# Kernel optimization log

Hardware: AMD Instinct MI355X
Metric: run time of the kernel (lower is better)

## Reference

```python
import math
import jax, jax.numpy as jnp
import numpy as np

HIDDEN = 2048
N_HEADS = 16
N_KV_HEADS = 4
HEAD_DIM = HIDDEN // N_HEADS  # 128
SEQ = 2048
BATCH = 2
RMS_EPS = 1.1920928955078125e-07  # torch float32 eps (nn.RMSNorm default eps=None)


def setup_inputs() -> dict:
    key = jax.random.key(0)
    ks = jax.random.split(key, 8)
    x = jax.random.normal(ks[0], (BATCH, SEQ, HIDDEN), dtype=jnp.float32)
    # RoPE tables, half-rotation layout: [f0..f_{d/2-1}, f0..f_{d/2-1}]
    inv_freq = 1.0 / (10000.0 ** (jnp.arange(0, HEAD_DIM, 2, dtype=jnp.float32) / HEAD_DIM))
    t = jnp.arange(SEQ, dtype=jnp.float32)
    freqs = jnp.outer(t, inv_freq)                      # [S, D/2]
    emb = jnp.concatenate([freqs, freqs], axis=-1)      # [S, D]
    sin, cos = jnp.sin(emb), jnp.cos(emb)
    s = 0.02
    Wq = jax.random.normal(ks[1], (HIDDEN, HIDDEN), dtype=jnp.float32) * s
    Wk = jax.random.normal(ks[2], (HIDDEN, N_KV_HEADS * HEAD_DIM), dtype=jnp.float32) * s
    Wv = jax.random.normal(ks[3], (HIDDEN, N_KV_HEADS * HEAD_DIM), dtype=jnp.float32) * s
    Wo = jax.random.normal(ks[4], (HIDDEN, HIDDEN), dtype=jnp.float32) * s
    q_norm_w = jnp.ones((HEAD_DIM,), dtype=jnp.float32)
    k_norm_w = jnp.ones((HEAD_DIM,), dtype=jnp.float32)
    return {"x": x, "sin": sin, "cos": cos, "Wq": Wq, "Wk": Wk, "Wv": Wv,
            "Wo": Wo, "q_norm_w": q_norm_w, "k_norm_w": k_norm_w}


def _rms_norm(t, w):
    # RMSNorm over last dim (head_dim) with learned weight
    var = jnp.mean(t * t, axis=-1, keepdims=True)
    return t * jax.lax.rsqrt(var + RMS_EPS) * w


def _apply_rope(t, sin, cos):
    # t: [B, H, S, D]; sin/cos: [S, D] broadcast
    half = t.shape[-1] // 2
    rotated = jnp.concatenate([-t[..., half:], t[..., :half]], axis=-1)
    return cos * t + sin * rotated


def reference(x, sin, cos, Wq, Wk, Wv, Wo, q_norm_w, k_norm_w):
    b, s, _ = x.shape
    rep = N_HEADS // N_KV_HEADS
    # Q: proj -> norm -> transpose -> rope
    q = (x @ Wq).reshape(b, s, N_HEADS, HEAD_DIM)
    q = _rms_norm(q, q_norm_w).transpose(0, 2, 1, 3)           # [B, H, S, D]
    q = _apply_rope(q, sin, cos)
    # K: proj -> repeat kv heads -> norm -> transpose -> rope
    k = (x @ Wk).reshape(b, s, N_KV_HEADS, HEAD_DIM)
    k = jnp.repeat(k, rep, axis=2)                              # [B, S, H, D]
    k = _rms_norm(k, k_norm_w).transpose(0, 2, 1, 3)            # [B, H, S, D]
    k = _apply_rope(k, sin, cos)
    # V: proj -> repeat kv heads -> transpose
    v = (x @ Wv).reshape(b, s, N_KV_HEADS, HEAD_DIM)
    v = jnp.repeat(v, rep, axis=2).transpose(0, 2, 1, 3)        # [B, H, S, D]
    # explicit masked softmax attention (materializes [B,H,S,S])
    scores = jnp.einsum('bhqd,bhkd->bhqk', q, k) / math.sqrt(HEAD_DIM)
    causal = jnp.triu(jnp.ones((s, s), dtype=bool), 1)
    scores = jnp.where(causal, -jnp.inf, scores)
    attn = jax.nn.softmax(scores, axis=-1)
    o = jnp.einsum('bhqk,bhkd->bhqd', attn, v)                  # [B, H, S, D]
    o = o.transpose(0, 2, 1, 3).reshape(b, s, HIDDEN)
    return o @ Wo
```

## Files before the change

### kernel.cpp

```cpp
#include <hip/hip_runtime.h>

typedef __attribute__((ext_vector_type(8))) short bf16x8;
typedef __attribute__((ext_vector_type(4))) short bf16x4;
typedef __attribute__((ext_vector_type(4))) float f32x4;

#define HIDDEN 2048
#define NH 16
#define NKV 4
#define HD 128
#define SEQ_N 2048
#define NT 4096
#define QKV_N 3072
#define RMS_EPS 1.1920928955078125e-07f
#define QSCALE 0.08838834764831845f
#define SM_C 12.0f

static __device__ __forceinline__ float b2f(unsigned short u) {
  union { unsigned int i; float f; } v; v.i = ((unsigned int)u) << 16; return v.f;
}
static __device__ __forceinline__ unsigned short f2b(float f) {
  union { float f; unsigned int i; } v; v.f = f;
  unsigned int r = (v.i + 0x7fffu + ((v.i >> 16) & 1u)) >> 16;
  return (unsigned short)r;
}
static __device__ __forceinline__ void gload_lds16(const unsigned short* g, unsigned short* l) {
  __builtin_amdgcn_global_load_lds(
      (const __attribute__((address_space(1))) unsigned int*)g,
      (__attribute__((address_space(3))) unsigned int*)l, 16, 0, 0);
}
static __device__ __forceinline__ void store_c(float* p, float v) { *p = v; }
static __device__ __forceinline__ void store_c(unsigned short* p, float v) { *p = f2b(v); }

template <typename OutT>
__device__ __forceinline__ void gemm_tile(
    const unsigned short* __restrict__ A, int lda,
    const unsigned short* __restrict__ BT, int ldb,
    OutT* __restrict__ C, int ldc,
    int K, int m0, int nloc0, int nout0) {
  __shared__ unsigned short As[4096], Bs[4096];
  const int tid  = threadIdx.x;
  const int wid  = tid >> 6, lane = tid & 63;
  const int g    = lane >> 4, cc = lane & 15;
  const int wr   = wid >> 1,  wc = wid & 1;
  const int r0   = tid >> 2;
  const int cb0  = (tid & 3) * 8;

  f32x4 acc[4][4];
#pragma unroll
  for (int i = 0; i < 4; ++i)
#pragma unroll
    for (int j = 0; j < 4; ++j) acc[i][j] = (f32x4){0.f, 0.f, 0.f, 0.f};

  unsigned short* AsW0 = As + wid * 512;
  unsigned short* AsW1 = As + 2048 + wid * 512;
  unsigned short* BsW0 = Bs + wid * 512;
  unsigned short* BsW1 = Bs + 2048 + wid * 512;
  const unsigned short* Ab0 = A  + (size_t)(m0 + r0)        * lda + cb0;
  const unsigned short* Ab1 = A  + (size_t)(m0 + 64 + r0)   * lda + cb0;
  const unsigned short* Bb0 = BT + (size_t)(nloc0 + r0)     * ldb + cb0;
  const unsigned short* Bb1 = BT + (size_t)(nloc0 + 64 + r0)* ldb + cb0;

  for (int kt = 0; kt < K; kt += 32) {
    gload_lds16(Ab0 + kt, AsW0);
    gload_lds16(Ab1 + kt, AsW1);
    gload_lds16(Bb0 + kt, BsW0);
    gload_lds16(Bb1 + kt, BsW1);
    __syncthreads();
    bf16x8 af[4], bfr[4];
#pragma unroll
    for (int mi = 0; mi < 4; ++mi)
      af[mi] = *(const bf16x8*)(As + ((wr * 64 + mi * 16 + cc) * 32 + g * 8));
#pragma unroll
    for (int ni = 0; ni < 4; ++ni)
      bfr[ni] = *(const bf16x8*)(Bs + ((wc * 64 + ni * 16 + cc) * 32 + g * 8));
#pragma unroll
    for (int mi = 0; mi < 4; ++mi)
#pragma unroll
      for (int ni = 0; ni < 4; ++ni)
        acc[mi][ni] = __builtin_amdgcn_mfma_f32_16x16x32_bf16(af[mi], bfr[ni], acc[mi][ni], 0, 0, 0);
    __syncthreads();
  }
#pragma unroll
  for (int mi = 0; mi < 4; ++mi)
#pragma unroll
    for (int ni = 0; ni < 4; ++ni)
#pragma unroll
      for (int j = 0; j < 4; ++j) {
        int row = m0 + wr * 64 + mi * 16 + g * 4 + j;
        int col = nout0 + wc * 64 + ni * 16 + cc;
        store_c(&C[(size_t)row * ldc + col], acc[mi][ni][j]);
      }
}

__global__ __launch_bounds__(256) void k_gemm_qkv(
    const unsigned short* __restrict__ x,
    const unsigned short* __restrict__ WqT,
    const unsigned short* __restrict__ WkT,
    const unsigned short* __restrict__ WvT,
    unsigned short* __restrict__ Praw) {
  int wg = (blockIdx.x & 7) * 96 + (blockIdx.x >> 3);
  int nb = wg % 24, mb = wg / 24;
  int n0 = nb * 128;
  const unsigned short* BT; int nloc;
  if (n0 < HIDDEN)            { BT = WqT; nloc = n0; }
  else if (n0 < HIDDEN + 512) { BT = WkT; nloc = n0 - HIDDEN; }
  else                        { BT = WvT; nloc = n0 - (HIDDEN + 512); }
  gemm_tile<unsigned short>(x, HIDDEN, BT, HIDDEN, Praw, QKV_N, HIDDEN, mb * 128, nloc, n0);
}

__global__ __launch_bounds__(256) void k_gemm_o(
    const unsigned short* __restrict__ Oa,
    const unsigned short* __restrict__ WoT,
    float* __restrict__ out) {
  int wg = (blockIdx.x & 7) * 64 + (blockIdx.x >> 3);
  int nb = wg % 16, mb = wg / 16;
  gemm_tile<float>(Oa, HIDDEN, WoT, HIDDEN, out, HIDDEN, HIDDEN, mb * 128, nb * 128, nb * 128);
}

__global__ __launch_bounds__(256) void k_cvt_f2b(
    const float* __restrict__ src, unsigned short* __restrict__ dst) {
  int i = (blockIdx.x * 256 + threadIdx.x) * 8;
  float4 a = *(const float4*)(src + i);
  float4 b = *(const float4*)(src + i + 4);
  bf16x8 v;
  v[0] = (short)f2b(a.x); v[1] = (short)f2b(a.y); v[2] = (short)f2b(a.z); v[3] = (short)f2b(a.w);
  v[4] = (short)f2b(b.x); v[5] = (short)f2b(b.y); v[6] = (short)f2b(b.z); v[7] = (short)f2b(b.w);
  *(bf16x8*)(dst + i) = v;
}

__global__ __launch_bounds__(256) void k_transpose_f2b(
    const float* __restrict__ src, unsigned short* __restrict__ dst,
    int ld_src, int ld_dst, int tilesC) {
  __shared__ float T[64][68];
  int tr = blockIdx.x / tilesC, tc = blockIdx.x % tilesC;
  int r0 = tr * 64, c0 = tc * 64;
  int tid = threadIdx.x;
#pragma unroll
  for (int it = 0; it < 4; ++it) {
    int u = it * 256 + tid;
    int r = u >> 4, cb = (u & 15) * 4;
    float4 v = *(const float4*)(src + (size_t)(r0 + r) * ld_src + c0 + cb);
    T[r][cb] = v.x; T[r][cb + 1] = v.y; T[r][cb + 2] = v.z; T[r][cb + 3] = v.w;
  }
  __syncthreads();
#pragma unroll
  for (int it = 0; it < 2; ++it) {
    int u = it * 256 + tid;
    int dc = u >> 3, rb = (u & 7) * 8;
    bf16x8 v;
#pragma unroll
    for (int j = 0; j < 8; ++j) v[j] = (short)f2b(T[rb + j][dc]);
    *(bf16x8*)(dst + (size_t)(c0 + dc) * ld_dst + r0 + rb) = v;
  }
}

__global__ __launch_bounds__(256) void k_transpose_bb(
    const unsigned short* __restrict__ src, unsigned short* __restrict__ dst,
    int ld_src, int ld_dst, int tilesC) {
  __shared__ unsigned short T[64][80];
  int tr = blockIdx.x / tilesC, tc = blockIdx.x % tilesC;
  int r0 = tr * 64, c0 = tc * 64;
  int tid = threadIdx.x;
#pragma unroll
  for (int it = 0; it < 2; ++it) {
    int u = it * 256 + tid; int r = u >> 3, cb = (u & 7) * 8;
    bf16x8 v = *(const bf16x8*)(src + (size_t)(r0 + r) * ld_src + c0 + cb);
    *(bf16x8*)(&T[r][cb]) = v;
  }
  __syncthreads();
#pragma unroll
  for (int it = 0; it < 2; ++it) {
    int u = it * 256 + tid; int dc = u >> 3, rb = (u & 7) * 8;
    bf16x8 v;
#pragma unroll
    for (int j = 0; j < 8; ++j) v[j] = (short)T[rb + j][dc];
    *(bf16x8*)(dst + (size_t)(c0 + dc) * ld_dst + r0 + rb) = v;
  }
}

__global__ __launch_bounds__(256) void k_qk_post(
    const unsigned short* __restrict__ Praw,
    const float* __restrict__ sinT,
    const float* __restrict__ cosT,
    const float* __restrict__ qw,
    const float* __restrict__ kw,
    unsigned short* __restrict__ Qbuf,
    unsigned short* __restrict__ Kbuf) {
  int sub = threadIdx.x >> 4;
  int sl  = threadIdx.x & 15;
  int rid = blockIdx.x * 16 + sub;
  int t = rid / 20, slot = rid - t * 20;
  int b = t >> 11, s = t & 2047;
  const int isq = (slot < 16);
  int cb = isq ? slot * 128 : HIDDEN + (slot - 16) * 128;
  const unsigned short* src = Praw + (size_t)t * QKV_N + cb;
  const int d0 = sl * 4;
  bf16x4 a0 = *(const bf16x4*)(src + d0);
  bf16x4 a1 = *(const bf16x4*)(src + 64 + d0);
  float x0[4], x1[4];
  float ssq = 0.f;
#pragma unroll
  for (int j = 0; j < 4; ++j) {
    x0[j] = b2f((unsigned short)a0[j]);
    x1[j] = b2f((unsigned short)a1[j]);
    ssq += x0[j] * x0[j] + x1[j] * x1[j];
  }
#pragma unroll
  for (int mk = 1; mk < 16; mk <<= 1) ssq += __shfl_xor(ssq, mk, 64);
  float r = rsqrtf(ssq * (1.0f / 128.0f) + RMS_EPS);
  const float* w = isq ? qw : kw;
  f32x4 w0 = *(const f32x4*)(w + d0);
  f32x4 w1 = *(const f32x4*)(w + 64 + d0);
  f32x4 cs0 = *(const f32x4*)(cosT + s * 128 + d0);
  f32x4 cs1 = *(const f32x4*)(cosT + s * 128 + 64 + d0);
  f32x4 sn0 = *(const f32x4*)(sinT + s * 128 + d0);
  f32x4 sn1 = *(const f32x4*)(sinT + s * 128 + 64 + d0);
  unsigned short* dst = isq
      ? Qbuf + ((size_t)(b * NH + slot) * SEQ_N + s) * HD
      : Kbuf + ((size_t)(b * NKV + (slot - 16)) * SEQ_N + s) * HD;
  const float qs = isq ? QSCALE : 1.0f;
  bf16x4 o0, o1;
#pragma unroll
  for (int j = 0; j < 4; ++j) {
    float n0 = x0[j] * r * w0[j];
    float n1 = x1[j] * r * w1[j];
    o0[j] = (short)f2b((cs0[j] * n0 - sn0[j] * n1) * qs);
    o1[j] = (short)f2b((cs1[j] * n1 + sn1[j] * n0) * qs);
  }
  *(bf16x4*)(dst + d0) = o0;
  *(bf16x4*)(dst + 64 + d0) = o1;
}

__global__ __launch_bounds__(256, 2) void k_attn(
    const unsigned short* __restrict__ Q,
    const unsigned short* __restrict__ K,
    const unsigned short* __restrict__ V,
    unsigned short* __restrict__ O) {
  __shared__ unsigned short Ks[2][64 * 128];
  __shared__ unsigned short Vs[2][128 * 64];
  __shared__ unsigned short Ps[4][16 * 64];
  const int tid = threadIdx.x, wid = tid >> 6, lane = tid & 63;
  const int g = lane >> 4, c = lane & 15;
  const int bid = blockIdx.x;
  const int bh = bid & 31;
  const int b = bh >> 4, h = bh & 15;
  const int z = bid >> 5;
  const int zz = z & 7, zr = z >> 3;
  const int qt = (zr == 0) ? zz : (zr == 1) ? 15 - zz : (zr == 2) ? 16 + zz : 31 - zz;
  const int wq0 = qt * 64 + wid * 16;
  const int kv = h >> 2;
  const int nt = qt + 1;

  const unsigned short* Qp = Q + (size_t)(b * NH + h) * SEQ_N * HD;
  const unsigned short* Kp = K + (size_t)(b * NKV + kv) * SEQ_N * HD;
  const unsigned short* Vp = V + (size_t)(kv * HD) * NT + b * SEQ_N;

  const int krow_l = lane >> 4;
  const int kcol_l = (lane & 15) * 8;
  const int vrow_l = lane >> 3;
  const int vcol_l = (lane & 7) * 8;

  bf16x8 qfr[4];
#pragma unroll
  for (int ks = 0; ks < 4; ++ks)
    qfr[ks] = *(const bf16x8*)(Qp + (size_t)(wq0 + c) * HD + ks * 32 + g * 8);

  f32x4 o[8];
#pragma unroll
  for (int df = 0; df < 8; ++df) o[df] = (f32x4){0.f, 0.f, 0.f, 0.f};
  float l_i[4] = {0.f, 0.f, 0.f, 0.f};

#define STAGE(BUF, KBASE)                                                          \
  {                                                                                \
    _Pragma("unroll")                                                              \
    for (int ch = 0; ch < 4; ++ch) {                                               \
      int chunk = wid * 4 + ch;                                                    \
      int rk = chunk * 4 + krow_l;                                                 \
      int ck = kcol_l ^ ((rk & 15) << 3);                                          \
      gload_lds16(Kp + (size_t)((KBASE) + rk) * HD + ck, &Ks[BUF][chunk * 512]);   \
      int rv = chunk * 8 + vrow_l;                                                 \
      int cv = vcol_l ^ ((rv & 7) << 3);                                           \
      gload_lds16(Vp + (size_t)rv * NT + (KBASE) + cv, &Vs[BUF][chunk * 512]);     \
    }                                                                              \
  }

  int buf = 0;
  STAGE(0, 0);
  __syncthreads();

  for (int kt = 0; kt < nt; ++kt) {
    const int kbase = kt * 64;
    if (kt + 1 < nt) STAGE(buf ^ 1, kbase + 64);

    f32x4 s[4];
#pragma unroll
    for (int kf = 0; kf < 4; ++kf) s[kf] = (f32x4){0.f, 0.f, 0.f, 0.f};
    __builtin_amdgcn_s_setprio(1);
#pragma unroll
    for (int ks = 0; ks < 4; ++ks) {
      bf16x8 bk[4];
#pragma unroll
      for (int kf = 0; kf < 4; ++kf) {
        int r = kf * 16 + c;
        int e = (ks * 32 + g * 8) ^ ((r & 15) << 3);
        bk[kf] = *(const bf16x8*)(&Ks[buf][r * 128 + e]);
      }
#pragma unroll
      for (int kf = 0; kf < 4; ++kf)
        s[kf] = __builtin_amdgcn_mfma_f32_16x16x32_bf16(qfr[ks], bk[kf], s[kf], 0, 0, 0);
    }
    __builtin_amdgcn_s_setprio(0);
    if (kbase + 63 > wq0) {
#pragma unroll
      for (int kf = 0; kf < 4; ++kf)
#pragma unroll
        for (int i = 0; i < 4; ++i) {
          int q = wq0 + g * 4 + i;
          int kp = kbase + kf * 16 + c;
          if (kp > q) s[kf][i] = -1e30f;
        }
    }
#pragma unroll
    for (int kf = 0; kf < 4; ++kf)
#pragma unroll
      for (int i = 0; i < 4; ++i) {
        float p = __expf(s[kf][i] - SM_C);
        l_i[i] += p;
        int r = g * 4 + i;
        int e = (kf * 16 + c) ^ ((r & 7) << 3);
        Ps[wid][r * 64 + e] = f2b(p);
      }
    __builtin_amdgcn_s_setprio(1);
#pragma unroll
    for (int ksp = 0; ksp < 2; ++ksp) {
      int ep = (ksp * 32 + g * 8) ^ ((c & 7) << 3);
      bf16x8 pa = *(const bf16x8*)(&Ps[wid][c * 64 + ep]);
#pragma unroll
      for (int df = 0; df < 8; ++df) {
        int rv = df * 16 + c;
        int e = (ksp * 32 + g * 8) ^ ((rv & 7) << 3);
        bf16x8 vb = *(const bf16x8*)(&Vs[buf][rv * 64 + e]);
        o[df] = __builtin_amdgcn_mfma_f32_16x16x32_bf16(pa, vb, o[df], 0, 0, 0);
      }
    }
    __builtin_amdgcn_s_setprio(0);
    __syncthreads();
    buf ^= 1;
  }

  unsigned short* Op = O + (size_t)(b * SEQ_N) * HIDDEN + h * HD;
#pragma unroll
  for (int i = 0; i < 4; ++i) {
    float t = l_i[i];
    t += __shfl_xor(t, 1, 64);
    t += __shfl_xor(t, 2, 64);
    t += __shfl_xor(t, 4, 64);
    t += __shfl_xor(t, 8, 64);
    float inv = 1.0f / t;
    int q = wq0 + g * 4 + i;
#pragma unroll
    for (int df = 0; df < 8; ++df)
      Op[(size_t)q * HIDDEN + df * 16 + c] = f2b(o[df][i] * inv);
  }
#undef STAGE
}

extern "C" void kernel_launch(void* const* d_in, const int* in_sizes, int n_in,
                              void* d_out, int out_size, void* d_ws, size_t ws_size,
                              hipStream_t stream) {
  const float* x    = (const float*)d_in[0];
  const float* sinT = (const float*)d_in[1];
  const float* cosT = (const float*)d_in[2];
  const float* Wq   = (const float*)d_in[3];
  const float* Wk   = (const float*)d_in[4];
  const float* Wv   = (const float*)d_in[5];
  const float* Wo   = (const float*)d_in[6];
  const float* qw   = (const float*)d_in[7];
  const float* kw   = (const float*)d_in[8];
  float* out = (float*)d_out;
  unsigned short* ws = (unsigned short*)d_ws;

  unsigned short* Xb   = ws;
  unsigned short* WqT  = ws + 8388608;
  unsigned short* WkT  = ws + 12582912;
  unsigned short* WvT  = ws + 13631488;
  unsigned short* WoT  = ws + 14680064;
  unsigned short* Praw = ws + 18874368;
  unsigned short* Qbuf = ws + 31457280;
  unsigned short* Kbuf = ws + 39845888;
  unsigned short* Vt   = ws + 41943040;
  unsigned short* Oatt = ws + 44040192;

  dim3 blk(256);
  k_cvt_f2b<<<4096, blk, 0, stream>>>(x, Xb);
  k_transpose_f2b<<<1024, blk, 0, stream>>>(Wq, WqT, 2048, 2048, 32);
  k_transpose_f2b<<<256,  blk, 0, stream>>>(Wk, WkT, 512,  2048, 8);
  k_transpose_f2b<<<256,  blk, 0, stream>>>(Wv, WvT, 512,  2048, 8);
  k_transpose_f2b<<<1024, blk, 0, stream>>>(Wo, WoT, 2048, 2048, 32);
  k_gemm_qkv<<<768, blk, 0, stream>>>(Xb, WqT, WkT, WvT, Praw);
  k_qk_post<<<5120, blk, 0, stream>>>(Praw, sinT, cosT, qw, kw, Qbuf, Kbuf);
  k_transpose_bb<<<512, blk, 0, stream>>>(Praw + 2560, Vt, 3072, 4096, 8);
  k_attn<<<1024, blk, 0, stream>>>(Qbuf, Kbuf, Vt, Oatt);
  k_gemm_o<<<512, blk, 0, stream>>>(Oatt, WoT, out);
}
```

Measured before the change: 321.0 us.

## Load K/V directly from global in attention, merge weight transposes, use exp2

The attention kernel drops its double-buffered LDS staging of K and V, along with the barriers and setprio hints, and reads MFMA operands straight from global memory through L1/L2. The four weight-transpose launches become one kernel that picks its matrix by block index. The softmax exponent is rewritten as exp2 of an FMA with log2(e) folded into the constants. Each attention operand load now goes to global memory, and four waves share each K/V tile, so the kernel depends more on cache hits and memory latency in exchange for dropping the LDS copies and barriers.

```diff
diff --git a/kernel.cpp b/kernel.cpp
--- a/kernel.cpp
+++ b/kernel.cpp
@@ -13,7 +13,8 @@
 #define QKV_N 3072
 #define RMS_EPS 1.1920928955078125e-07f
 #define QSCALE 0.08838834764831845f
-#define SM_C 12.0f
+#define SM_L2E 1.4426950408889634f
+#define SM_C2  17.312340490667562f
 
 static __device__ __forceinline__ float b2f(unsigned short u) {
   union { unsigned int i; float f; } v; v.i = ((unsigned int)u) << 16; return v.f;
@@ -128,11 +129,20 @@
   *(bf16x8*)(dst + i) = v;
 }
 
-__global__ __launch_bounds__(256) void k_transpose_f2b(
-    const float* __restrict__ src, unsigned short* __restrict__ dst,
-    int ld_src, int ld_dst, int tilesC) {
+__global__ __launch_bounds__(256) void k_transpose_all(
+    const float* __restrict__ Wq, const float* __restrict__ Wk,
+    const float* __restrict__ Wv, const float* __restrict__ Wo,
+    unsigned short* __restrict__ WqT, unsigned short* __restrict__ WkT,
+    unsigned short* __restrict__ WvT, unsigned short* __restrict__ WoT) {
   __shared__ float T[64][68];
-  int tr = blockIdx.x / tilesC, tc = blockIdx.x % tilesC;
+  int bid = blockIdx.x;
+  const float* src; unsigned short* dst; int ld_src, tilesC, tile;
+  if (bid < 1024)      { src = Wq; dst = WqT; ld_src = 2048; tilesC = 32; tile = bid; }
+  else if (bid < 1280) { src = Wk; dst = WkT; ld_src = 512;  tilesC = 8;  tile = bid - 1024; }
+  else if (bid < 1536) { src = Wv; dst = WvT; ld_src = 512;  tilesC = 8;  tile = bid - 1280; }
+  else                 { src = Wo; dst = WoT; ld_src = 2048; tilesC = 32; tile = bid - 1536; }
+  const int ld_dst = 2048;
+  int tr = tile / tilesC, tc = tile % tilesC;
   int r0 = tr * 64, c0 = tc * 64;
   int tid = threadIdx.x;
 #pragma unroll
@@ -231,13 +241,11 @@
   *(bf16x4*)(dst + 64 + d0) = o1;
 }
 
-__global__ __launch_bounds__(256, 2) void k_attn(
+__global__ __launch_bounds__(256) void k_attn(
     const unsigned short* __restrict__ Q,
     const unsigned short* __restrict__ K,
     const unsigned short* __restrict__ V,
     unsigned short* __restrict__ O) {
-  __shared__ unsigned short Ks[2][64 * 128];
-  __shared__ unsigned short Vs[2][128 * 64];
   __shared__ unsigned short Ps[4][16 * 64];
   const int tid = threadIdx.x, wid = tid >> 6, lane = tid & 63;
   const int g = lane >> 4, c = lane & 15;
@@ -255,11 +263,6 @@
   const unsigned short* Kp = K + (size_t)(b * NKV + kv) * SEQ_N * HD;
   const unsigned short* Vp = V + (size_t)(kv * HD) * NT + b * SEQ_N;
 
-  const int krow_l = lane >> 4;
-  const int kcol_l = (lane & 15) * 8;
-  const int vrow_l = lane >> 3;
-  const int vcol_l = (lane & 7) * 8;
-
   bf16x8 qfr[4];
 #pragma unroll
   for (int ks = 0; ks < 4; ++ks)
@@ -270,46 +273,22 @@
   for (int df = 0; df < 8; ++df) o[df] = (f32x4){0.f, 0.f, 0.f, 0.f};
   float l_i[4] = {0.f, 0.f, 0.f, 0.f};
 
-#define STAGE(BUF, KBASE)                                                          \
-  {                                                                                \
-    _Pragma("unroll")                                                              \
-    for (int ch = 0; ch < 4; ++ch) {                                               \
-      int chunk = wid * 4 + ch;                                                    \
-      int rk = chunk * 4 + krow_l;                                                 \
-      int ck = kcol_l ^ ((rk & 15) << 3);                                          \
-      gload_lds16(Kp + (size_t)((KBASE) + rk) * HD + ck, &Ks[BUF][chunk * 512]);   \
-      int rv = chunk * 8 + vrow_l;                                                 \
-      int cv = vcol_l ^ ((rv & 7) << 3);                                           \
-      gload_lds16(Vp + (size_t)rv * NT + (KBASE) + cv, &Vs[BUF][chunk * 512]);     \
-    }                                                                              \
-  }
-
-  int buf = 0;
-  STAGE(0, 0);
-  __syncthreads();
-
   for (int kt = 0; kt < nt; ++kt) {
     const int kbase = kt * 64;
-    if (kt + 1 < nt) STAGE(buf ^ 1, kbase + 64);
 
     f32x4 s[4];
 #pragma unroll
     for (int kf = 0; kf < 4; ++kf) s[kf] = (f32x4){0.f, 0.f, 0.f, 0.f};
-    __builtin_amdgcn_s_setprio(1);
 #pragma unroll
     for (int ks = 0; ks < 4; ++ks) {
       bf16x8 bk[4];
 #pragma unroll
-      for (int kf = 0; kf < 4; ++kf) {
-        int r = kf * 16 + c;
-        int e = (ks * 32 + g * 8) ^ ((r & 15) << 3);
-        bk[kf] = *(const bf16x8*)(&Ks[buf][r * 128 + e]);
-      }
+      for (int kf = 0; kf < 4; ++kf)
+        bk[kf] = *(const bf16x8*)(Kp + (size_t)(kbase + kf * 16 + c) * HD + ks * 32 + g * 8);
 #pragma unroll
       for (int kf = 0; kf < 4; ++kf)
         s[kf] = __builtin_amdgcn_mfma_f32_16x16x32_bf16(qfr[ks], bk[kf], s[kf], 0, 0, 0);
     }
-    __builtin_amdgcn_s_setprio(0);
     if (kbase + 63 > wq0) {
 #pragma unroll
       for (int kf = 0; kf < 4; ++kf)
@@ -324,28 +303,22 @@
     for (int kf = 0; kf < 4; ++kf)
 #pragma unroll
       for (int i = 0; i < 4; ++i) {
-        float p = __expf(s[kf][i] - SM_C);
+        float p = exp2f(fmaf(s[kf][i], SM_L2E, -SM_C2));
         l_i[i] += p;
         int r = g * 4 + i;
         int e = (kf * 16 + c) ^ ((r & 7) << 3);
         Ps[wid][r * 64 + e] = f2b(p);
       }
-    __builtin_amdgcn_s_setprio(1);
 #pragma unroll
     for (int ksp = 0; ksp < 2; ++ksp) {
       int ep = (ksp * 32 + g * 8) ^ ((c & 7) << 3);
       bf16x8 pa = *(const bf16x8*)(&Ps[wid][c * 64 + ep]);
 #pragma unroll
       for (int df = 0; df < 8; ++df) {
-        int rv = df * 16 + c;
-        int e = (ksp * 32 + g * 8) ^ ((rv & 7) << 3);
-        bf16x8 vb = *(const bf16x8*)(&Vs[buf][rv * 64 + e]);
+        bf16x8 vb = *(const bf16x8*)(Vp + (size_t)(df * 16 + c) * NT + kbase + ksp * 32 + g * 8);
         o[df] = __builtin_amdgcn_mfma_f32_16x16x32_bf16(pa, vb, o[df], 0, 0, 0);
       }
     }
-    __builtin_amdgcn_s_setprio(0);
-    __syncthreads();
-    buf ^= 1;
   }
 
   unsigned short* Op = O + (size_t)(b * SEQ_N) * HIDDEN + h * HD;
@@ -362,7 +335,6 @@
     for (int df = 0; df < 8; ++df)
       Op[(size_t)q * HIDDEN + df * 16 + c] = f2b(o[df][i] * inv);
   }
-#undef STAGE
 }
 
 extern "C" void kernel_launch(void* const* d_in, const int* in_sizes, int n_in,
@@ -393,10 +365,7 @@
 
   dim3 blk(256);
   k_cvt_f2b<<<4096, blk, 0, stream>>>(x, Xb);
-  k_transpose_f2b<<<1024, blk, 0, stream>>>(Wq, WqT, 2048, 2048, 32);
-  k_transpose_f2b<<<256,  blk, 0, stream>>>(Wk, WkT, 512,  2048, 8);
-  k_transpose_f2b<<<256,  blk, 0, stream>>>(Wv, WvT, 512,  2048, 8);
-  k_transpose_f2b<<<1024, blk, 0, stream>>>(Wo, WoT, 2048, 2048, 32);
+  k_transpose_all<<<2560, blk, 0, stream>>>(Wq, Wk, Wv, Wo, WqT, WkT, WvT, WoT);
   k_gemm_qkv<<<768, blk, 0, stream>>>(Xb, WqT, WkT, WvT, Praw);
   k_qk_post<<<5120, blk, 0, stream>>>(Praw, sinT, cosT, qw, kw, Qbuf, Kbuf);
   k_transpose_bb<<<512, blk, 0, stream>>>(Praw + 2560, Vt, 3072, 4096, 8);
```

Result: slower. 503.5 us (+56.9%).
